# Optimization experiments

Measured on AMD Instinct MI355X. Metric: run time of the kernel, lower is better.

The kernel has to match this reference:

```python
import jax, jax.numpy as jnp
import numpy as np

B, N, DK = 16, 2048, 512

def setup_inputs() -> dict:
    key = jax.random.key(0)
    k1, k2, k3, k4 = jax.random.split(key, 4)
    return {
        'src_embedding': jax.random.normal(k1, (B, N, DK), dtype=jnp.float32),
        'target_embedding': jax.random.normal(k2, (B, N, DK), dtype=jnp.float32),
        'src': jax.random.normal(k3, (B, N, 3), dtype=jnp.float32),
        'target': jax.random.normal(k4, (B, N, 3), dtype=jnp.float32),
    }

def reference(src_embedding, target_embedding, src, target):
    d_k = src_embedding.shape[2]
    # attention-weighted soft correspondence: [B, N, M]
    scores = jnp.einsum('bnd,bmd->bnm', src_embedding, target_embedding)
    scores = jax.nn.softmax(scores / jnp.sqrt(jnp.asarray(d_k, scores.dtype)), axis=2)
    tgt_corr = jnp.einsum('bnm,bmc->bnc', scores, src)            # [B, N, 3]
    tgt_mean = jnp.mean(target, axis=1, keepdims=True)            # [B, 1, 3]
    corr_mean = jnp.mean(tgt_corr, axis=1, keepdims=True)         # [B, 1, 3]
    # cross-covariance H = (target - mu_t)^T @ (tgt_corr - mu_c): [B, 3, 3]
    H = jnp.einsum('bnc,bnd->bcd', target - tgt_mean, tgt_corr - corr_mean)
    U, S, Vh = jnp.linalg.svd(H)                                  # H = U diag(S) Vh
    det = jnp.linalg.det(jnp.matmul(U, Vh))                       # [B]
    # C = diag(1, 1, det) reflection fix; R = U @ C @ Vh
    diag = jnp.stack([jnp.ones_like(det), jnp.ones_like(det), det], axis=-1)  # [B, 3]
    R = jnp.matmul(U * diag[:, None, :], Vh)                      # [B, 3, 3]
    # t^T = mu_t^T - R @ mu_c^T, returned as [B, 1, 3]
    t = tgt_mean - jnp.einsum('bij,bkj->bki', R, corr_mean)
    return (R, t)
```

## Files before the change

kernel.cpp:

```cpp
#include <hip/hip_runtime.h>
#include <hip/hip_bf16.h>
#include <stdint.h>


#define B_  16
#define N_  2048
#define DK_ 512
#define SCALE 0.044194173824159216f

typedef __bf16 bf16x8 __attribute__((ext_vector_type(8)));
typedef float  f32x16 __attribute__((ext_vector_type(16)));
typedef float  f32x4  __attribute__((ext_vector_type(4)));

union BF8 { bf16x8 v; unsigned u[4]; };

__device__ inline unsigned pkbf(float a, float b) {
  unsigned r;
  asm("v_cvt_pk_bf16_f32 %0, %1, %2" : "=v"(r) : "v"(a), "v"(b));
  return r;
}

__device__ inline void gl_lds16(const void* g, void* l) {
  __builtin_amdgcn_global_load_lds(
      (const __attribute__((address_space(1))) unsigned int*)g,
      (__attribute__((address_space(3))) unsigned int*)l, 16, 0, 0);
}

__global__ __launch_bounds__(256)
void cvt_k_kernel(const float* __restrict__ in, uint4* __restrict__ out)
{
  const size_t total = (size_t)B_ * N_ * DK_ / 8;
  for (size_t i = (size_t)blockIdx.x * 256 + threadIdx.x; i < total;
       i += (size_t)gridDim.x * 256) {
    f32x4 a = ((const f32x4*)in)[2 * i];
    f32x4 c = ((const f32x4*)in)[2 * i + 1];
    uint4 w;
    w.x = pkbf(a[0], a[1]);
    w.y = pkbf(a[2], a[3]);
    w.z = pkbf(c[0], c[1]);
    w.w = pkbf(c[2], c[3]);
    out[i] = w;
  }
}

__global__ __launch_bounds__(512, 2)
void attn_stats_kernel(const float* __restrict__ Q,
                       const unsigned char* __restrict__ Kbf,
                       const float* __restrict__ Vsrc, float* __restrict__ part)
{
  __shared__ __align__(16) unsigned char s_k[2][32 * 1024];
  __shared__ __align__(16) float s_srcT[3 * 1024];

  const int L   = blockIdx.x;
  const int xcd = L & 7;
  const int kk  = L >> 3;
  const int b   = xcd + 8 * (kk & 1);
  const int ms  = (kk >> 1) & 1;
  const int nb  = kk >> 2;

  const int tid  = threadIdx.x;
  const int lane = tid & 63;
  const int wid  = tid >> 6;
  const int row  = lane & 31;
  const int hi   = lane >> 5;

  const int mchunk0 = ms * 1024;

  {
    const float* vp = Vsrc + ((size_t)b * N_ + mchunk0) * 3;
    for (int idx = tid; idx < 3072; idx += 512) {
      int m = idx / 3, c = idx - 3 * m;
      s_srcT[c * 1024 + m] = vp[idx];
    }
  }

  const int qglob = nb * 256 + wid * 32 + row;
  BF8 qf[32];
  {
    const f32x4* qp = (const f32x4*)(Q + ((size_t)b * N_ + qglob) * DK_);
    #pragma unroll
    for (int t = 0; t < 32; ++t) {
      f32x4 f0 = qp[t * 4 + hi * 2];
      f32x4 f1 = qp[t * 4 + hi * 2 + 1];
      qf[t].u[0] = pkbf(f0[0], f0[1]);
      qf[t].u[1] = pkbf(f0[2], f0[3]);
      qf[t].u[2] = pkbf(f1[0], f1[1]);
      qf[t].u[3] = pkbf(f1[2], f1[3]);
    }
  }

  const unsigned char* kbase = Kbf + ((size_t)b * N_ + mchunk0) * (DK_ * 2);

  #define STAGE(bb, t)                                                       \
    { _Pragma("unroll")                                                      \
      for (int j = 0; j < 4; ++j) {                                          \
        const int r_ = wid * 4 + j;                                          \
        gl_lds16(kbase + (((size_t)(t) * 32 + r_) << 10)                     \
                       + (unsigned)((lane ^ r_) << 4),                       \
                 &s_k[bb][r_ << 10]);                                        \
      } }

  float lsum = 0.f, a0 = 0.f, a1 = 0.f, a2 = 0.f;

  const unsigned kread_base = (unsigned)(row * 1024);
  const unsigned kread_xor  = (unsigned)(row << 4);

  STAGE(0, 0)
  __syncthreads();

  for (int tile = 0; tile < 32; ++tile) {
    const int cur = tile & 1;
    if (tile + 1 < 32) STAGE(cur ^ 1, tile + 1)

    const unsigned char* bp = &s_k[cur][0];
    f32x16 sc0, sc1;
    #pragma unroll
    for (int i = 0; i < 16; ++i) { sc0[i] = 0.f; sc1[i] = 0.f; }
    __builtin_amdgcn_s_setprio(1);
    #pragma unroll
    for (int t = 0; t < 32; t += 2) {
      BF8 kf0, kf1;
      kf0.v = *(const bf16x8*)(bp + kread_base +
                (((unsigned)(t * 32 + hi * 16)) ^ kread_xor));
      sc0 = __builtin_amdgcn_mfma_f32_32x32x16_bf16(kf0.v, qf[t].v, sc0, 0, 0, 0);
      kf1.v = *(const bf16x8*)(bp + kread_base +
                (((unsigned)((t + 1) * 32 + hi * 16)) ^ kread_xor));
      sc1 = __builtin_amdgcn_mfma_f32_32x32x16_bf16(kf1.v, qf[t + 1].v, sc1, 0, 0, 0);
    }
    __builtin_amdgcn_s_setprio(0);

    #pragma unroll
    for (int j = 0; j < 4; ++j) {
      const int mrun = tile * 32 + j * 8 + hi * 4;
      f32x4 s0 = *(const f32x4*)&s_srcT[mrun];
      f32x4 s1 = *(const f32x4*)&s_srcT[1024 + mrun];
      f32x4 s2 = *(const f32x4*)&s_srcT[2048 + mrun];
      #pragma unroll
      for (int i2 = 0; i2 < 4; ++i2) {
        float w = __expf((sc0[j * 4 + i2] + sc1[j * 4 + i2]) * SCALE);
        lsum += w;
        a0 += w * s0[i2];
        a1 += w * s1[i2];
        a2 += w * s2[i2];
      }
    }

    __syncthreads();
  }
  #undef STAGE

  a0   += __shfl_xor(a0, 32);
  a1   += __shfl_xor(a1, 32);
  a2   += __shfl_xor(a2, 32);
  lsum += __shfl_xor(lsum, 32);

  if (hi == 0) {
    f32x4 o; o[0] = a0; o[1] = a1; o[2] = a2; o[3] = lsum;
    *(f32x4*)(part + (((size_t)ms * B_ + b) * N_ + qglob) * 4) = o;
  }
}

__global__ __launch_bounds__(512, 2)
void attn_stats_f32_kernel(const float* __restrict__ Q, const float* __restrict__ K,
                           const float* __restrict__ Vsrc, float* __restrict__ part)
{
  __shared__ __align__(16) unsigned char s_k[32 * 1024];
  __shared__ __align__(16) float s_srcT[3 * 1024];

  const int L   = blockIdx.x;
  const int xcd = L & 7;
  const int kk  = L >> 3;
  const int b   = xcd + 8 * (kk & 1);
  const int ms  = (kk >> 1) & 1;
  const int nb  = kk >> 2;

  const int tid  = threadIdx.x;
  const int lane = tid & 63;
  const int wid  = tid >> 6;
  const int row  = lane & 31;
  const int hi   = lane >> 5;

  const int mchunk0 = ms * 1024;

  {
    const float* vp = Vsrc + ((size_t)b * N_ + mchunk0) * 3;
    for (int idx = tid; idx < 3072; idx += 512) {
      int m = idx / 3, c = idx - 3 * m;
      s_srcT[c * 1024 + m] = vp[idx];
    }
  }

  const int qglob = nb * 256 + wid * 32 + row;
  BF8 qf[32];
  {
    const f32x4* qp = (const f32x4*)(Q + ((size_t)b * N_ + qglob) * DK_);
    #pragma unroll
    for (int t = 0; t < 32; ++t) {
      f32x4 f0 = qp[t * 4 + hi * 2];
      f32x4 f1 = qp[t * 4 + hi * 2 + 1];
      qf[t].u[0] = pkbf(f0[0], f0[1]);
      qf[t].u[1] = pkbf(f0[2], f0[3]);
      qf[t].u[2] = pkbf(f1[0], f1[1]);
      qf[t].u[3] = pkbf(f1[2], f1[3]);
    }
  }

  const f32x4* kg = (const f32x4*)(K + ((size_t)b * N_ + mchunk0) * DK_);

  float lsum = 0.f, a0 = 0.f, a1 = 0.f, a2 = 0.f;

  f32x4 stg[8];
  #pragma unroll
  for (int i = 0; i < 8; ++i) stg[i] = kg[i * 512 + tid];

  const unsigned kread_base = (unsigned)(row * 1024);
  const unsigned kread_xor  = (unsigned)(row << 4);

  for (int tile = 0; tile < 32; ++tile) {
    __syncthreads();
    #pragma unroll
    for (int i = 0; i < 8; ++i) {
      int idx  = i * 512 + tid;
      int r    = idx >> 7;
      int colb = (idx & 127) * 8;
      unsigned addr = (unsigned)(r * 1024) + ((unsigned)colb ^ ((unsigned)(r << 4)));
      uint2 w2;
      w2.x = pkbf(stg[i][0], stg[i][1]);
      w2.y = pkbf(stg[i][2], stg[i][3]);
      *(uint2*)(s_k + addr) = w2;
    }
    __syncthreads();
    if (tile + 1 < 32) {
      const f32x4* kt = kg + (size_t)(tile + 1) * 4096;
      #pragma unroll
      for (int i = 0; i < 8; ++i) stg[i] = kt[i * 512 + tid];
    }
    f32x16 sc0, sc1;
    #pragma unroll
    for (int i = 0; i < 16; ++i) { sc0[i] = 0.f; sc1[i] = 0.f; }
    __builtin_amdgcn_s_setprio(1);
    #pragma unroll
    for (int t = 0; t < 32; t += 2) {
      BF8 kf0, kf1;
      kf0.v = *(const bf16x8*)(s_k + kread_base +
                (((unsigned)(t * 32 + hi * 16)) ^ kread_xor));
      sc0 = __builtin_amdgcn_mfma_f32_32x32x16_bf16(kf0.v, qf[t].v, sc0, 0, 0, 0);
      kf1.v = *(const bf16x8*)(s_k + kread_base +
                (((unsigned)((t + 1) * 32 + hi * 16)) ^ kread_xor));
      sc1 = __builtin_amdgcn_mfma_f32_32x32x16_bf16(kf1.v, qf[t + 1].v, sc1, 0, 0, 0);
    }
    __builtin_amdgcn_s_setprio(0);
    #pragma unroll
    for (int j = 0; j < 4; ++j) {
      const int mrun = tile * 32 + j * 8 + hi * 4;
      f32x4 s0 = *(const f32x4*)&s_srcT[mrun];
      f32x4 s1 = *(const f32x4*)&s_srcT[1024 + mrun];
      f32x4 s2 = *(const f32x4*)&s_srcT[2048 + mrun];
      #pragma unroll
      for (int i2 = 0; i2 < 4; ++i2) {
        float w = __expf((sc0[j * 4 + i2] + sc1[j * 4 + i2]) * SCALE);
        lsum += w;
        a0 += w * s0[i2];
        a1 += w * s1[i2];
        a2 += w * s2[i2];
      }
    }
  }

  a0   += __shfl_xor(a0, 32);
  a1   += __shfl_xor(a1, 32);
  a2   += __shfl_xor(a2, 32);
  lsum += __shfl_xor(lsum, 32);

  if (hi == 0) {
    f32x4 o; o[0] = a0; o[1] = a1; o[2] = a2; o[3] = lsum;
    *(f32x4*)(part + (((size_t)ms * B_ + b) * N_ + qglob) * 4) = o;
  }
}

__global__ void reduce_kernel(const float* __restrict__ part,
                              const float* __restrict__ tgt,
                              float* __restrict__ ws2)
{
  const int b = blockIdx.x, tid = threadIdx.x;
  float s[15];
  #pragma unroll
  for (int j = 0; j < 15; ++j) s[j] = 0.f;

  for (int n = tid; n < N_; n += 256) {
    f32x4 p0 = *(const f32x4*)(part + (((size_t)0 * B_ + b) * N_ + n) * 4);
    f32x4 p1 = *(const f32x4*)(part + (((size_t)1 * B_ + b) * N_ + n) * 4);
    float inv = 1.0f / (p0[3] + p1[3]);
    float c0 = (p0[0] + p1[0]) * inv;
    float c1 = (p0[1] + p1[1]) * inv;
    float c2 = (p0[2] + p1[2]) * inv;
    const float* tp = tgt + ((size_t)b * N_ + n) * 3;
    float t0 = tp[0], t1 = tp[1], t2 = tp[2];
    s[0] += t0;  s[1] += t1;  s[2] += t2;
    s[3] += c0;  s[4] += c1;  s[5] += c2;
    s[6] += t0 * c0;  s[7]  += t0 * c1;  s[8]  += t0 * c2;
    s[9] += t1 * c0;  s[10] += t1 * c1;  s[11] += t1 * c2;
    s[12] += t2 * c0; s[13] += t2 * c1;  s[14] += t2 * c2;
  }
  #pragma unroll
  for (int j = 0; j < 15; ++j) {
    #pragma unroll
    for (int off = 32; off > 0; off >>= 1) s[j] += __shfl_xor(s[j], off);
  }
  __shared__ float red[4][15];
  int lane = tid & 63, w = tid >> 6;
  if (lane == 0) {
    #pragma unroll
    for (int j = 0; j < 15; ++j) red[w][j] = s[j];
  }
  __syncthreads();
  if (tid < 15)
    ws2[b * 16 + tid] = red[0][tid] + red[1][tid] + red[2][tid] + red[3][tid];
}

__device__ inline void jrot(double A[3][3], double V[3][3], int p, int q) {
  double apq = A[p][q];
  if (fabs(apq) < 1e-300) return;
  double tau = (A[q][q] - A[p][p]) / (2.0 * apq);
  double tt = (tau >= 0.0) ? 1.0 / (tau + sqrt(1.0 + tau * tau))
                           : 1.0 / (tau - sqrt(1.0 + tau * tau));
  double c = 1.0 / sqrt(1.0 + tt * tt), sn = tt * c;
  for (int k = 0; k < 3; ++k) {
    double akp = A[k][p], akq = A[k][q];
    A[k][p] = c * akp - sn * akq;
    A[k][q] = sn * akp + c * akq;
  }
  for (int k = 0; k < 3; ++k) {
    double apk = A[p][k], aqk = A[q][k];
    A[p][k] = c * apk - sn * aqk;
    A[q][k] = sn * apk + c * aqk;
  }
  for (int k = 0; k < 3; ++k) {
    double vkp = V[k][p], vkq = V[k][q];
    V[k][p] = c * vkp - sn * vkq;
    V[k][q] = sn * vkp + c * vkq;
  }
}

__global__ void svd_kernel(const float* __restrict__ ws2, float* __restrict__ out)
{
  const int b = threadIdx.x;
  if (b >= B_) return;
  const float* s = ws2 + b * 16;
  const double invN = 1.0 / (double)N_;
  double stv[3] = {s[0], s[1], s[2]};
  double scv[3] = {s[3], s[4], s[5]};
  double H[3][3];
  for (int c = 0; c < 3; ++c)
    for (int d = 0; d < 3; ++d)
      H[c][d] = (double)s[6 + c * 3 + d] - stv[c] * scv[d] * invN;

  double A[3][3], V[3][3] = {{1,0,0},{0,1,0},{0,0,1}};
  for (int i = 0; i < 3; ++i)
    for (int j = 0; j < 3; ++j) {
      double acc = 0.0;
      for (int c = 0; c < 3; ++c) acc += H[c][i] * H[c][j];
      A[i][j] = acc;
    }
  for (int sw = 0; sw < 15; ++sw) { jrot(A,V,0,1); jrot(A,V,0,2); jrot(A,V,1,2); }

  double e[3] = {A[0][0], A[1][1], A[2][2]};
  double vc[3][3];
  for (int k = 0; k < 3; ++k)
    for (int i = 0; i < 3; ++i) vc[k][i] = V[i][k];
  for (int a2 = 0; a2 < 2; ++a2)
    for (int b2 = 0; b2 < 2 - a2; ++b2)
      if (e[b2] < e[b2 + 1]) {
        double te = e[b2]; e[b2] = e[b2 + 1]; e[b2 + 1] = te;
        for (int i = 0; i < 3; ++i) {
          double tv = vc[b2][i]; vc[b2][i] = vc[b2 + 1][i]; vc[b2 + 1][i] = tv;
        }
      }

  double u1[3], u2[3], u3[3];
  for (int i = 0; i < 3; ++i)
    u1[i] = H[i][0]*vc[0][0] + H[i][1]*vc[0][1] + H[i][2]*vc[0][2];
  double n1 = sqrt(u1[0]*u1[0] + u1[1]*u1[1] + u1[2]*u1[2]);
  n1 = fmax(n1, 1e-300);
  for (int i = 0; i < 3; ++i) u1[i] /= n1;
  for (int i = 0; i < 3; ++i)
    u2[i] = H[i][0]*vc[1][0] + H[i][1]*vc[1][1] + H[i][2]*vc[1][2];
  double d12 = u1[0]*u2[0] + u1[1]*u2[1] + u1[2]*u2[2];
  for (int i = 0; i < 3; ++i) u2[i] -= d12 * u1[i];
  double n2 = sqrt(u2[0]*u2[0] + u2[1]*u2[1] + u2[2]*u2[2]);
  n2 = fmax(n2, 1e-300);
  for (int i = 0; i < 3; ++i) u2[i] /= n2;
  u3[0] = u1[1]*u2[2] - u1[2]*u2[1];
  u3[1] = u1[2]*u2[0] - u1[0]*u2[2];
  u3[2] = u1[0]*u2[1] - u1[1]*u2[0];

  double detV = vc[0][0]*(vc[1][1]*vc[2][2] - vc[1][2]*vc[2][1])
              - vc[0][1]*(vc[1][0]*vc[2][2] - vc[1][2]*vc[2][0])
              + vc[0][2]*(vc[1][0]*vc[2][1] - vc[1][1]*vc[2][0]);

  double R[3][3];
  for (int i = 0; i < 3; ++i)
    for (int j = 0; j < 3; ++j)
      R[i][j] = u1[i]*vc[0][j] + u2[i]*vc[1][j] + detV * u3[i]*vc[2][j];

  for (int i = 0; i < 3; ++i)
    for (int j = 0; j < 3; ++j)
      out[b * 9 + i * 3 + j] = (float)R[i][j];

  double muc[3] = {scv[0]*invN, scv[1]*invN, scv[2]*invN};
  for (int i = 0; i < 3; ++i) {
    double ti = stv[i]*invN - (R[i][0]*muc[0] + R[i][1]*muc[1] + R[i][2]*muc[2]);
    out[B_ * 9 + b * 3 + i] = (float)ti;
  }
}

extern "C" void kernel_launch(void* const* d_in, const int* in_sizes, int n_in,
                              void* d_out, int out_size, void* d_ws, size_t ws_size,
                              hipStream_t stream)
{
  const float* srcE = (const float*)d_in[0];
  const float* tgtE = (const float*)d_in[1];
  const float* srcP = (const float*)d_in[2];
  const float* tgtP = (const float*)d_in[3];
  float* out = (float*)d_out;

  const size_t kbf_bytes   = (size_t)B_ * N_ * DK_ * 2;
  const size_t part_floats = (size_t)2 * B_ * N_ * 4;

  if (ws_size >= kbf_bytes + part_floats * 4 + 1024) {
    unsigned char* kbf = (unsigned char*)d_ws;
    float* part = (float*)(kbf + kbf_bytes);
    float* ws2  = part + part_floats;
    cvt_k_kernel<<<dim3(2048), dim3(256), 0, stream>>>(tgtE, (uint4*)kbf);
    attn_stats_kernel<<<dim3(256), dim3(512), 0, stream>>>(srcE, kbf, srcP, part);
    reduce_kernel<<<dim3(B_), dim3(256), 0, stream>>>(part, tgtP, ws2);
    svd_kernel<<<dim3(1), dim3(64), 0, stream>>>(ws2, out);
  } else {
    float* part = (float*)d_ws;
    float* ws2  = part + part_floats;
    attn_stats_f32_kernel<<<dim3(256), dim3(512), 0, stream>>>(srcE, tgtE, srcP, part);
    reduce_kernel<<<dim3(B_), dim3(256), 0, stream>>>(part, tgtP, ws2);
    svd_kernel<<<dim3(1), dim3(64), 0, stream>>>(ws2, out);
  }
}
```

Before: 131.8 us.

## Software-pipeline QK MFMA with previous tile's exp/accumulate epilogue

Restructures the tile loop into a two-stage software pipeline with ping-pong score accumulators, so the MFMA score computation for the next tile interleaves with the exp and weighted accumulation of the previous tile. The goal is to hide transcendental and VALU epilogue latency behind matrix-core work. It also replaces __expf with exp2f using a pre-multiplied log2e scale. The cost is doubled accumulator registers, which may raise register pressure and lower occupancy.

```diff
diff --git a/kernel.cpp b/kernel.cpp
--- a/kernel.cpp
+++ b/kernel.cpp
@@ -6,7 +6,8 @@
 #define B_  16
 #define N_  2048
 #define DK_ 512
-#define SCALE 0.044194173824159216f
+#define SCALE  0.044194173824159216f
+#define SCALE2 0.063758709f
 
 typedef __bf16 bf16x8 __attribute__((ext_vector_type(8)));
 typedef float  f32x16 __attribute__((ext_vector_type(16)));
@@ -105,49 +106,80 @@
   const unsigned kread_base = (unsigned)(row * 1024);
   const unsigned kread_xor  = (unsigned)(row << 4);
 
+  #define MF8(bp, X0, X1, tb)                                                \
+    { _Pragma("unroll")                                                      \
+      for (int t = (tb); t < (tb) + 8; t += 2) {                             \
+        BF8 kf0, kf1;                                                        \
+        kf0.v = *(const bf16x8*)((bp) + kread_base +                         \
+                  (((unsigned)(t * 32 + hi * 16)) ^ kread_xor));             \
+        X0 = __builtin_amdgcn_mfma_f32_32x32x16_bf16(kf0.v, qf[t].v, X0, 0, 0, 0); \
+        kf1.v = *(const bf16x8*)((bp) + kread_base +                         \
+                  (((unsigned)((t + 1) * 32 + hi * 16)) ^ kread_xor));       \
+        X1 = __builtin_amdgcn_mfma_f32_32x32x16_bf16(kf1.v, qf[t + 1].v, X1, 0, 0, 0); \
+      } }
+
+  #define EPI4(P0, P1, mtp, j)                                               \
+    { const int mrun = (mtp) * 32 + (j) * 8 + hi * 4;                        \
+      f32x4 s0 = *(const f32x4*)&s_srcT[mrun];                               \
+      f32x4 s1 = *(const f32x4*)&s_srcT[1024 + mrun];                        \
+      f32x4 s2 = *(const f32x4*)&s_srcT[2048 + mrun];                        \
+      _Pragma("unroll")                                                      \
+      for (int i2 = 0; i2 < 4; ++i2) {                                       \
+        float w = exp2f((P0[(j) * 4 + i2] + P1[(j) * 4 + i2]) * SCALE2);     \
+        lsum += w;                                                           \
+        a0 += w * s0[i2];                                                    \
+        a1 += w * s1[i2];                                                    \
+        a2 += w * s2[i2];                                                    \
+      } }
+
+  #define TILE_BODY(bp, C0, C1, P0, P1, mtp)                                 \
+    { _Pragma("unroll")                                                      \
+      for (int i = 0; i < 16; ++i) { C0[i] = 0.f; C1[i] = 0.f; }             \
+      __builtin_amdgcn_s_setprio(1);                                         \
+      MF8(bp, C0, C1, 0)  EPI4(P0, P1, mtp, 0)                               \
+      MF8(bp, C0, C1, 8)  EPI4(P0, P1, mtp, 1)                               \
+      MF8(bp, C0, C1, 16) EPI4(P0, P1, mtp, 2)                               \
+      MF8(bp, C0, C1, 24) EPI4(P0, P1, mtp, 3)                               \
+      __builtin_amdgcn_s_setprio(0); }
+
+  const unsigned char* bp0 = &s_k[0][0];
+  const unsigned char* bp1 = &s_k[1][0];
+  f32x16 A0, A1, B0, B1;
+
   STAGE(0, 0)
   __syncthreads();
 
-  for (int tile = 0; tile < 32; ++tile) {
-    const int cur = tile & 1;
-    if (tile + 1 < 32) STAGE(cur ^ 1, tile + 1)
-
-    const unsigned char* bp = &s_k[cur][0];
-    f32x16 sc0, sc1;
-    #pragma unroll
-    for (int i = 0; i < 16; ++i) { sc0[i] = 0.f; sc1[i] = 0.f; }
+  STAGE(1, 1)
+  {
+    #pragma unroll
+    for (int i = 0; i < 16; ++i) { A0[i] = 0.f; A1[i] = 0.f; }
     __builtin_amdgcn_s_setprio(1);
-    #pragma unroll
-    for (int t = 0; t < 32; t += 2) {
-      BF8 kf0, kf1;
-      kf0.v = *(const bf16x8*)(bp + kread_base +
-                (((unsigned)(t * 32 + hi * 16)) ^ kread_xor));
-      sc0 = __builtin_amdgcn_mfma_f32_32x32x16_bf16(kf0.v, qf[t].v, sc0, 0, 0, 0);
-      kf1.v = *(const bf16x8*)(bp + kread_base +
-                (((unsigned)((t + 1) * 32 + hi * 16)) ^ kread_xor));
-      sc1 = __builtin_amdgcn_mfma_f32_32x32x16_bf16(kf1.v, qf[t + 1].v, sc1, 0, 0, 0);
-    }
+    MF8(bp0, A0, A1, 0)
+    MF8(bp0, A0, A1, 8)
+    MF8(bp0, A0, A1, 16)
+    MF8(bp0, A0, A1, 24)
     __builtin_amdgcn_s_setprio(0);
-
-    #pragma unroll
-    for (int j = 0; j < 4; ++j) {
-      const int mrun = tile * 32 + j * 8 + hi * 4;
-      f32x4 s0 = *(const f32x4*)&s_srcT[mrun];
-      f32x4 s1 = *(const f32x4*)&s_srcT[1024 + mrun];
-      f32x4 s2 = *(const f32x4*)&s_srcT[2048 + mrun];
-      #pragma unroll
-      for (int i2 = 0; i2 < 4; ++i2) {
-        float w = __expf((sc0[j * 4 + i2] + sc1[j * 4 + i2]) * SCALE);
-        lsum += w;
-        a0 += w * s0[i2];
-        a1 += w * s1[i2];
-        a2 += w * s2[i2];
-      }
-    }
-
+  }
+  __syncthreads();
+
+  for (int p = 0; p < 15; ++p) {
+    STAGE(0, 2 * p + 2)
+    TILE_BODY(bp1, B0, B1, A0, A1, 2 * p)
     __syncthreads();
-  }
+    STAGE(1, 2 * p + 3)
+    TILE_BODY(bp0, A0, A1, B0, B1, 2 * p + 1)
+    __syncthreads();
+  }
+  TILE_BODY(bp1, B0, B1, A0, A1, 30)
+  EPI4(B0, B1, 31, 0)
+  EPI4(B0, B1, 31, 1)
+  EPI4(B0, B1, 31, 2)
+  EPI4(B0, B1, 31, 3)
+
   #undef STAGE
+  #undef MF8
+  #undef EPI4
+  #undef TILE_BODY
 
   a0   += __shfl_xor(a0, 32);
   a1   += __shfl_xor(a1, 32);
```

New measurement: 238.3 us. +80.8%, slower.
